# Performance work log

Measured on AMD Instinct MI355X. Metric: run time of the kernel, lower is better.

The kernel has to match this reference:

```python
import jax, jax.numpy as jnp
import numpy as np

INPUT_DIM, QK_DIM, V_DIM = 1024, 512, 512

def setup_inputs() -> dict:
    key = jax.random.key(0)
    ks = jax.random.split(key, 7)
    B, S = 4, 2048
    scale = 1.0 / np.sqrt(INPUT_DIM)
    return {
        "x": jax.random.normal(ks[0], (B, S, INPUT_DIM), dtype=jnp.float32),
        "Wq": jax.random.normal(ks[1], (INPUT_DIM, QK_DIM), dtype=jnp.float32) * scale,
        "bq": jax.random.normal(ks[2], (QK_DIM,), dtype=jnp.float32) * 0.01,
        "Wk": jax.random.normal(ks[3], (INPUT_DIM, QK_DIM), dtype=jnp.float32) * scale,
        "bk": jax.random.normal(ks[4], (QK_DIM,), dtype=jnp.float32) * 0.01,
        "Wv": jax.random.normal(ks[5], (INPUT_DIM, V_DIM), dtype=jnp.float32) * scale,
        "bv": jax.random.normal(ks[6], (V_DIM,), dtype=jnp.float32) * 0.01,
    }

def reference(x, Wq, bq, Wk, bk, Wv, bv):
    # q,k: (B,S,Dqk), v: (B,S,Dv)
    q = jnp.einsum("bsi,id->bsd", x, Wq) + bq
    k = jnp.einsum("bsi,id->bsd", x, Wk) + bk
    v = jnp.einsum("bsi,id->bsd", x, Wv) + bv
    scale = 1.0 / jnp.sqrt(jnp.asarray(q.shape[-1], q.dtype))
    scores = jnp.einsum("bqd,bkd->bqk", q, k) * scale  # (B,S,S)
    attn = jax.nn.softmax(scores, axis=-1)
    return jnp.einsum("bqk,bkd->bqd", attn, v)
```

## Files before the change

kernel.cpp:

```cpp
#include <hip/hip_runtime.h>

typedef __attribute__((ext_vector_type(8))) short short8;
typedef __attribute__((ext_vector_type(4))) float f32x4;

#define S_    2048
#define DI    1024
#define DQK   512
#define DV    512
#define NTOK  8192

#define GLL(gp, lp) __builtin_amdgcn_global_load_lds( \
    (const __attribute__((address_space(1))) unsigned int*)(gp), \
    (__attribute__((address_space(3))) unsigned int*)(lp), 16, 0, 0)

static __device__ __forceinline__ unsigned short f2bf(float f) {
  unsigned int u = __float_as_uint(f);
  u += 0x7fffu + ((u >> 16) & 1u);
  return (unsigned short)(u >> 16);
}

__global__ void conv_x_kernel(const float* __restrict__ x,
                              unsigned short* __restrict__ xb, int n) {
  int idx = (blockIdx.x * 256 + threadIdx.x) * 8;
  if (idx >= n) return;
  const float4* p = (const float4*)(x + idx);
  float4 f0 = p[0], f1 = p[1];
  uint4 o;
  o.x = (unsigned)f2bf(f0.x) | ((unsigned)f2bf(f0.y) << 16);
  o.y = (unsigned)f2bf(f0.z) | ((unsigned)f2bf(f0.w) << 16);
  o.z = (unsigned)f2bf(f1.x) | ((unsigned)f2bf(f1.y) << 16);
  o.w = (unsigned)f2bf(f1.z) | ((unsigned)f2bf(f1.w) << 16);
  *(uint4*)(xb + idx) = o;
}

__global__ void conv_wT_kernel(const float* __restrict__ W0, const float* __restrict__ W1,
                               const float* __restrict__ W2,
                               unsigned short* __restrict__ T0, unsigned short* __restrict__ T1,
                               unsigned short* __restrict__ T2,
                               float* __restrict__ rowsum) {
  __shared__ float tile[32][33];
  int mat = blockIdx.z;
  if (mat == 0 && blockIdx.x == 0)
    rowsum[blockIdx.y * 256 + threadIdx.x] = 0.f;
  const float* W = (mat == 0) ? W0 : (mat == 1) ? W1 : W2;
  unsigned short* T = (mat == 0) ? T0 : (mat == 1) ? T1 : T2;
  int n0 = blockIdx.x * 32, k0 = blockIdx.y * 32;
  int c = threadIdx.x & 31, r0 = threadIdx.x >> 5;
  for (int i = 0; i < 4; ++i) {
    int kk = r0 + i * 8;
    tile[kk][c] = W[(k0 + kk) * DQK + n0 + c];
  }
  __syncthreads();
  for (int i = 0; i < 4; ++i) {
    int nn = r0 + i * 8;
    T[(n0 + nn) * DI + k0 + c] = f2bf(tile[c][nn]);
  }
}

__device__ __forceinline__ void gemm_core_128x128(
    const unsigned short* __restrict__ A, const unsigned short* __restrict__ B,
    int lda, int ldb, int K, int m0, int n0,
    unsigned short* As, unsigned short* Bs, f32x4 (&acc)[4][4]) {
  int tid = threadIdx.x, lane = tid & 63, wv = tid >> 6;
  int quad = lane >> 4, l16 = lane & 15;
  int wm = wv >> 1, wn = wv & 1;
  int r0 = wv * 32 + (lane >> 2), c8 = (lane & 3) * 8;
  const unsigned short* ga0 = A + (size_t)(m0 + r0) * lda + c8;
  const unsigned short* ga1 = ga0 + (size_t)16 * lda;
  const unsigned short* gb0 = B + (size_t)(n0 + r0) * ldb + c8;
  const unsigned short* gb1 = gb0 + (size_t)16 * ldb;
  unsigned short* la0 = As + (wv * 32) * 32;
  unsigned short* la1 = la0 + 16 * 32;
  unsigned short* lb0 = Bs + (wv * 32) * 32;
  unsigned short* lb1 = lb0 + 16 * 32;
#pragma unroll
  for (int i = 0; i < 4; ++i)
#pragma unroll
    for (int j = 0; j < 4; ++j) acc[i][j] = (f32x4){0.f, 0.f, 0.f, 0.f};

  for (int k0 = 0; k0 < K; k0 += 32) {
    __syncthreads();
    GLL(ga0 + k0, la0);
    GLL(ga1 + k0, la1);
    GLL(gb0 + k0, lb0);
    GLL(gb1 + k0, lb1);
    __syncthreads();
    short8 af[4], bf[4];
#pragma unroll
    for (int t = 0; t < 4; ++t) {
      af[t] = *(const short8*)(As + (wm * 64 + t * 16 + l16) * 32 + quad * 8);
      bf[t] = *(const short8*)(Bs + (wn * 64 + t * 16 + l16) * 32 + quad * 8);
    }
#pragma unroll
    for (int tm = 0; tm < 4; ++tm)
#pragma unroll
      for (int tn = 0; tn < 4; ++tn)
        acc[tm][tn] = __builtin_amdgcn_mfma_f32_16x16x32_bf16(af[tm], bf[tn], acc[tm][tn], 0, 0, 0);
  }
}

__global__ __launch_bounds__(256, 2) void qkv_dma_kernel(
    const unsigned short* __restrict__ xb,
    const unsigned short* __restrict__ wqt, const unsigned short* __restrict__ wkt,
    const unsigned short* __restrict__ wvt,
    const float* __restrict__ bq, const float* __restrict__ bk, const float* __restrict__ bv,
    unsigned short* __restrict__ qo, unsigned short* __restrict__ ko,
    unsigned short* __restrict__ vto) {
  __shared__ unsigned short As[128 * 32];
  __shared__ unsigned short Bs[128 * 32];
  int bidx = blockIdx.x;
  int xcd = bidx & 7;
  int local = bidx >> 3;
  int mlocal = local & 7;
  int col12 = local >> 3;
  int mat = col12 >> 2;
  int m0 = (xcd * 8 + mlocal) * 128;
  int n0 = (col12 & 3) * 128;
  const unsigned short* wt = (mat == 0) ? wqt : (mat == 1) ? wkt : wvt;
  const float* bias = (mat == 0) ? bq : (mat == 1) ? bk : bv;
  float oscale = (mat == 0) ? 0.04419417382415922f : 1.0f;
  f32x4 acc[4][4];
  gemm_core_128x128(xb, wt, DI, DI, DI, m0, n0, As, Bs, acc);

  int tid = threadIdx.x, lane = tid & 63, wv = tid >> 6;
  int quad = lane >> 4, l16 = lane & 15;
  int wm = wv >> 1, wn = wv & 1;
  bool transp = (mat == 2);
  unsigned short* outp = (mat == 0) ? qo : (mat == 1) ? ko : vto;
#pragma unroll
  for (int tn = 0; tn < 4; ++tn) {
    int col = n0 + wn * 64 + tn * 16 + l16;
    float bc = bias[col];
#pragma unroll
    for (int tm = 0; tm < 4; ++tm) {
      int rowb = m0 + wm * 64 + tm * 16 + quad * 4;
      f32x4 a = acc[tm][tn];
      if (!transp) {
        outp[(size_t)(rowb + 0) * DQK + col] = f2bf((a.x + bc) * oscale);
        outp[(size_t)(rowb + 1) * DQK + col] = f2bf((a.y + bc) * oscale);
        outp[(size_t)(rowb + 2) * DQK + col] = f2bf((a.z + bc) * oscale);
        outp[(size_t)(rowb + 3) * DQK + col] = f2bf((a.w + bc) * oscale);
      } else {
        ushort4 pk;
        pk.x = f2bf(a.x + bc); pk.y = f2bf(a.y + bc);
        pk.z = f2bf(a.z + bc); pk.w = f2bf(a.w + bc);
        *(ushort4*)(outp + (size_t)col * NTOK + rowb) = pk;
      }
    }
  }
}

__global__ __launch_bounds__(256, 2) void s_exp_kernel(
    const unsigned short* __restrict__ q, const unsigned short* __restrict__ k,
    unsigned short* __restrict__ sp, float* __restrict__ rowsum) {
  __shared__ unsigned short As[128 * 32];
  __shared__ unsigned short Bs[128 * 32];
  int bidx = blockIdx.x;
  int xcd = bidx & 7, b = xcd >> 1;
  int sub = ((bidx >> 3) << 1) | (xcd & 1);
  int m0 = (sub >> 4) * 128, n0 = (sub & 15) * 128;
  f32x4 acc[4][4];
  gemm_core_128x128(q + (size_t)b * S_ * DQK, k + (size_t)b * S_ * DQK,
                    DQK, DQK, DQK, m0, n0, As, Bs, acc);

  int tid = threadIdx.x, lane = tid & 63, wv = tid >> 6;
  int quad = lane >> 4, l16 = lane & 15;
  int wm = wv >> 1, wn = wv & 1;
  unsigned short* Cb = sp + (size_t)b * S_ * S_;
#pragma unroll
  for (int tm = 0; tm < 4; ++tm) {
    int rowb = m0 + wm * 64 + tm * 16 + quad * 4;
    float rs[4] = {0.f, 0.f, 0.f, 0.f};
#pragma unroll
    for (int tn = 0; tn < 4; ++tn) {
      int col = n0 + wn * 64 + tn * 16 + l16;
      f32x4 a = acc[tm][tn];
      float e0 = __expf(a.x), e1 = __expf(a.y), e2 = __expf(a.z), e3 = __expf(a.w);
      Cb[(size_t)(rowb + 0) * S_ + col] = f2bf(e0);
      Cb[(size_t)(rowb + 1) * S_ + col] = f2bf(e1);
      Cb[(size_t)(rowb + 2) * S_ + col] = f2bf(e2);
      Cb[(size_t)(rowb + 3) * S_ + col] = f2bf(e3);
      rs[0] += e0; rs[1] += e1; rs[2] += e2; rs[3] += e3;
    }
    for (int off = 1; off < 16; off <<= 1)
#pragma unroll
      for (int r = 0; r < 4; ++r) rs[r] += __shfl_xor(rs[r], off);
    if (l16 == 0)
#pragma unroll
      for (int r = 0; r < 4; ++r) atomicAdd(rowsum + b * S_ + rowb + r, rs[r]);
  }
}

__global__ __launch_bounds__(256, 4) void pv_kernel(
    const unsigned short* __restrict__ sp, const unsigned short* __restrict__ vt,
    const float* __restrict__ rowsum, float* __restrict__ out) {
  __shared__ unsigned short As[2][64 * 64];
  __shared__ unsigned short Bs[2][64 * 64];
  int bidx = blockIdx.x;
  int xcd = bidx & 7, b = xcd >> 1;
  int sub = ((bidx >> 3) << 1) | (xcd & 1);
  int m0 = (sub >> 3) * 64, n0 = (sub & 7) * 64;
  int tid = threadIdx.x, lane = tid & 63, wv = tid >> 6;
  int quad = lane >> 4, l16 = lane & 15;
  int wm = wv >> 1, wn = wv & 1;
  const unsigned short* A = sp + (size_t)b * S_ * S_;
  const unsigned short* B = vt + (size_t)b * S_;

  int srow = tid >> 3;
  int schunk = (tid & 7) ^ (srow & 7);
  const unsigned short* gA0 = A + (size_t)(m0 + srow) * S_ + schunk * 8;
  const unsigned short* gA1 = A + (size_t)(m0 + 32 + srow) * S_ + schunk * 8;
  const unsigned short* gB0 = B + (size_t)(n0 + srow) * NTOK + schunk * 8;
  const unsigned short* gB1 = B + (size_t)(n0 + 32 + srow) * NTOK + schunk * 8;
  int ldsw0 = (wv * 8) * 64;
  int ldsw1 = (32 + wv * 8) * 64;

  f32x4 acc[2][2];
#pragma unroll
  for (int i = 0; i < 2; ++i)
#pragma unroll
    for (int j = 0; j < 2; ++j) acc[i][j] = (f32x4){0.f, 0.f, 0.f, 0.f};

  auto stage = [&](int buf, int k0) {
    GLL(gA0 + k0, &As[buf][ldsw0]);
    GLL(gA1 + k0, &As[buf][ldsw1]);
    GLL(gB0 + k0, &Bs[buf][ldsw0]);
    GLL(gB1 + k0, &Bs[buf][ldsw1]);
  };

  stage(0, 0);
  for (int kt = 0; kt < 32; ++kt) {
    int cur = kt & 1;
    __syncthreads();
    if (kt + 1 < 32) stage(cur ^ 1, (kt + 1) * 64);
#pragma unroll
    for (int ks = 0; ks < 2; ++ks) {
      int pc = ((ks * 4 + quad) ^ (l16 & 7)) * 8;
      short8 af[2], bf[2];
#pragma unroll
      for (int t = 0; t < 2; ++t) {
        af[t] = *(const short8*)(&As[cur][(wm * 32 + t * 16 + l16) * 64 + pc]);
        bf[t] = *(const short8*)(&Bs[cur][(wn * 32 + t * 16 + l16) * 64 + pc]);
      }
#pragma unroll
      for (int tm = 0; tm < 2; ++tm)
#pragma unroll
        for (int tn = 0; tn < 2; ++tn)
          acc[tm][tn] = __builtin_amdgcn_mfma_f32_16x16x32_bf16(af[tm], bf[tn], acc[tm][tn], 0, 0, 0);
    }
  }

  float* ob = out + (size_t)b * S_ * DV;
#pragma unroll
  for (int tm = 0; tm < 2; ++tm) {
    int rowb = m0 + wm * 32 + tm * 16 + quad * 4;
    float inv[4];
#pragma unroll
    for (int i = 0; i < 4; ++i) inv[i] = 1.0f / rowsum[b * S_ + rowb + i];
#pragma unroll
    for (int tn = 0; tn < 2; ++tn) {
      int col = n0 + wn * 32 + tn * 16 + l16;
      f32x4 a = acc[tm][tn];
      ob[(size_t)(rowb + 0) * DV + col] = a.x * inv[0];
      ob[(size_t)(rowb + 1) * DV + col] = a.y * inv[1];
      ob[(size_t)(rowb + 2) * DV + col] = a.z * inv[2];
      ob[(size_t)(rowb + 3) * DV + col] = a.w * inv[3];
    }
  }
}

extern "C" void kernel_launch(void* const* d_in, const int* in_sizes, int n_in,
                              void* d_out, int out_size, void* d_ws, size_t ws_size,
                              hipStream_t stream) {
  const float* x  = (const float*)d_in[0];
  const float* Wq = (const float*)d_in[1];
  const float* bq = (const float*)d_in[2];
  const float* Wk = (const float*)d_in[3];
  const float* bk = (const float*)d_in[4];
  const float* Wv = (const float*)d_in[5];
  const float* bv = (const float*)d_in[6];
  float* out = (float*)d_out;

  char* ws = (char*)d_ws;
  unsigned short* xb  = (unsigned short*)(ws);
  unsigned short* wqt = (unsigned short*)(ws + 16777216);
  unsigned short* wkt = (unsigned short*)(ws + 16777216 + 1048576);
  unsigned short* wvt = (unsigned short*)(ws + 16777216 + 2097152);
  unsigned short* qo  = (unsigned short*)(ws + 19922944);
  unsigned short* ko  = (unsigned short*)(ws + 19922944 + 8388608);
  unsigned short* vto = (unsigned short*)(ws + 19922944 + 16777216);
  unsigned short* sp  = (unsigned short*)(ws + 45088768);
  float* rowsum       = (float*)(ws + 45088768 + 33554432);

  conv_x_kernel<<<4096, 256, 0, stream>>>(x, xb, NTOK * DI);
  dim3 gw(16, 32, 3);
  conv_wT_kernel<<<gw, 256, 0, stream>>>(Wq, Wk, Wv, wqt, wkt, wvt, rowsum);
  qkv_dma_kernel<<<768, 256, 0, stream>>>(xb, wqt, wkt, wvt, bq, bk, bv, qo, ko, vto);
  s_exp_kernel<<<1024, 256, 0, stream>>>(qo, ko, sp, rowsum);
  pv_kernel<<<1024, 256, 0, stream>>>(sp, vto, rowsum, out);
}
```

Before: 180.8 us.

## Double-buffer LDS tiles in the GEMM core and XOR-swizzle LDS chunks

The shared 128x128 GEMM core now keeps two LDS buffers, so the global_load_lds for the next K-tile is issued before the MFMAs on the current tile. This removes one barrier per iteration and is meant to overlap global-to-LDS transfer with matrix math. The 16-byte column chunks are also XOR-swizzled by row, both in the global source address and in the LDS read offset, to reduce LDS bank conflicts on the fragment reads. Each block's LDS use doubles, which may cut occupancy. Overlap also depends on the compiler not inserting a full vmcnt wait before the LDS reads.

```diff
diff --git a/kernel.cpp b/kernel.cpp
--- a/kernel.cpp
+++ b/kernel.cpp
@@ -64,32 +64,42 @@
   int tid = threadIdx.x, lane = tid & 63, wv = tid >> 6;
   int quad = lane >> 4, l16 = lane & 15;
   int wm = wv >> 1, wn = wv & 1;
-  int r0 = wv * 32 + (lane >> 2), c8 = (lane & 3) * 8;
+  int r0 = wv * 32 + (lane >> 2);
+  int c8 = ((lane & 3) ^ ((lane >> 2) & 3)) * 8;
   const unsigned short* ga0 = A + (size_t)(m0 + r0) * lda + c8;
   const unsigned short* ga1 = ga0 + (size_t)16 * lda;
   const unsigned short* gb0 = B + (size_t)(n0 + r0) * ldb + c8;
   const unsigned short* gb1 = gb0 + (size_t)16 * ldb;
-  unsigned short* la0 = As + (wv * 32) * 32;
-  unsigned short* la1 = la0 + 16 * 32;
-  unsigned short* lb0 = Bs + (wv * 32) * 32;
-  unsigned short* lb1 = lb0 + 16 * 32;
+  int ldsw0 = (wv * 32) * 32;
+  int ldsw1 = ldsw0 + 16 * 32;
 #pragma unroll
   for (int i = 0; i < 4; ++i)
 #pragma unroll
     for (int j = 0; j < 4; ++j) acc[i][j] = (f32x4){0.f, 0.f, 0.f, 0.f};
 
-  for (int k0 = 0; k0 < K; k0 += 32) {
+  auto stage = [&](int buf, int k0) {
+    unsigned short* Ad = As + buf * (128 * 32);
+    unsigned short* Bd = Bs + buf * (128 * 32);
+    GLL(ga0 + k0, Ad + ldsw0);
+    GLL(ga1 + k0, Ad + ldsw1);
+    GLL(gb0 + k0, Bd + ldsw0);
+    GLL(gb1 + k0, Bd + ldsw1);
+  };
+
+  int nk = K >> 5;
+  int pc = (quad ^ (l16 & 3)) * 8;
+  stage(0, 0);
+  for (int kt = 0; kt < nk; ++kt) {
+    int cur = kt & 1;
     __syncthreads();
-    GLL(ga0 + k0, la0);
-    GLL(ga1 + k0, la1);
-    GLL(gb0 + k0, lb0);
-    GLL(gb1 + k0, lb1);
-    __syncthreads();
+    if (kt + 1 < nk) stage(cur ^ 1, (kt + 1) * 32);
+    const unsigned short* Ab = As + cur * (128 * 32);
+    const unsigned short* Bb = Bs + cur * (128 * 32);
     short8 af[4], bf[4];
 #pragma unroll
     for (int t = 0; t < 4; ++t) {
-      af[t] = *(const short8*)(As + (wm * 64 + t * 16 + l16) * 32 + quad * 8);
-      bf[t] = *(const short8*)(Bs + (wn * 64 + t * 16 + l16) * 32 + quad * 8);
+      af[t] = *(const short8*)(Ab + (wm * 64 + t * 16 + l16) * 32 + pc);
+      bf[t] = *(const short8*)(Bb + (wn * 64 + t * 16 + l16) * 32 + pc);
     }
 #pragma unroll
     for (int tm = 0; tm < 4; ++tm)
@@ -106,8 +116,8 @@
     const float* __restrict__ bq, const float* __restrict__ bk, const float* __restrict__ bv,
     unsigned short* __restrict__ qo, unsigned short* __restrict__ ko,
     unsigned short* __restrict__ vto) {
-  __shared__ unsigned short As[128 * 32];
-  __shared__ unsigned short Bs[128 * 32];
+  __shared__ unsigned short As[2 * 128 * 32];
+  __shared__ unsigned short Bs[2 * 128 * 32];
   int bidx = blockIdx.x;
   int xcd = bidx & 7;
   int local = bidx >> 3;
@@ -153,8 +163,8 @@
 __global__ __launch_bounds__(256, 2) void s_exp_kernel(
     const unsigned short* __restrict__ q, const unsigned short* __restrict__ k,
     unsigned short* __restrict__ sp, float* __restrict__ rowsum) {
-  __shared__ unsigned short As[128 * 32];
-  __shared__ unsigned short Bs[128 * 32];
+  __shared__ unsigned short As[2 * 128 * 32];
+  __shared__ unsigned short Bs[2 * 128 * 32];
   int bidx = blockIdx.x;
   int xcd = bidx & 7, b = xcd >> 1;
   int sub = ((bidx >> 3) << 1) | (xcd & 1);
```

After: 186.8 us. +3.3%, slower.
